# Kernel optimization log

Hardware: AMD Instinct MI355X
Metric: run time of the kernel (lower is better)

The kernel has to match this reference:

```python
import jax, jax.numpy as jnp
import numpy as np

N = 8192      # n_nodes == nfeat (square feature matrix, required by final Linear)
NHID = 64
NCLASS = 8
E = N * 32    # avg degree 32


def setup_inputs() -> dict:
    key = jax.random.key(0)
    ks = jax.random.split(key, 12)
    s = 1.0 / np.sqrt(NHID)
    return {
        "x": jax.random.normal(ks[0], (N, N), dtype=jnp.float32),
        "adj_row": jax.random.randint(ks[1], (E,), 0, N, dtype=jnp.int32),
        "adj_col": jax.random.randint(ks[2], (E,), 0, N, dtype=jnp.int32),
        "adj_val": jax.random.uniform(ks[3], (E,), dtype=jnp.float32),
        "W1": jax.random.uniform(ks[4], (N, NHID), minval=-s, maxval=s, dtype=jnp.float32),
        "b1": jax.random.uniform(ks[5], (NHID,), minval=-s, maxval=s, dtype=jnp.float32),
        "W2": jax.random.uniform(ks[6], (NHID, NHID), minval=-s, maxval=s, dtype=jnp.float32),
        "b2": jax.random.uniform(ks[7], (NHID,), minval=-s, maxval=s, dtype=jnp.float32),
        "W3": jax.random.uniform(ks[8], (NHID, NCLASS), minval=-s, maxval=s, dtype=jnp.float32),
        "b3": jax.random.uniform(ks[9], (NCLASS,), minval=-s, maxval=s, dtype=jnp.float32),
        "Wlin": jax.random.normal(ks[10], (1, N), dtype=jnp.float32) * (1.0 / np.sqrt(N)),
        "blin": jax.random.normal(ks[11], (1,), dtype=jnp.float32) * 0.01,
    }


def _gcn_layer(h, W, b, row, col, val):
    # support = h @ W ; out = spmm(adj, support) + b
    support = h @ W                              # [N, F_out]
    msgs = val[:, None] * support[col]           # gather source rows, scale by edge value
    out = jax.ops.segment_sum(msgs, row, num_segments=N)  # scatter-add into dest rows
    return out + b


def reference(x, adj_row, adj_col, adj_val, W1, b1, W2, b2, W3, b3, Wlin, blin):
    h = jax.nn.relu(_gcn_layer(x, W1, b1, adj_row, adj_col, adj_val))
    # dropout inactive (eval mode)
    h = jax.nn.relu(_gcn_layer(h, W2, b2, adj_row, adj_col, adj_val))
    h = _gcn_layer(h, W3, b3, adj_row, adj_col, adj_val)   # [N, NCLASS]
    h = jax.nn.log_softmax(h, axis=1)
    # LinearLayer(nfeat->1) applied to h^T [NCLASS, N] -> [NCLASS, 1], then transpose
    y = h.T @ Wlin.T + blin                      # [NCLASS, 1]
    return y.T                                   # [1, NCLASS]
```

## Files before the change

### kernel.cpp

```cpp
#include <hip/hip_runtime.h>

#define NN 8192
#define NHID 64
#define NCLASS 8
#define NEDGE (NN * 32)
#define NSPLIT 8
#define DEGCAP 128

typedef __attribute__((ext_vector_type(8))) short bf16x8_t;
typedef __attribute__((ext_vector_type(4))) float f32x4_t;

__device__ __forceinline__ unsigned short f2bf(float f) {
    unsigned int u = __float_as_uint(f);
    u += 0x7FFF + ((u >> 16) & 1);
    return (unsigned short)(u >> 16);
}

__global__ __launch_bounds__(256) void prep_kernel(const float* __restrict__ W1,
                                                   unsigned short* __restrict__ w1t,
                                                   const int* __restrict__ row,
                                                   const int* __restrict__ col,
                                                   const float* __restrict__ val,
                                                   int* __restrict__ cnt,
                                                   int* __restrict__ ccol,
                                                   float* __restrict__ cval) {
    const int bid = blockIdx.x;
    if (bid < 2048) {
        const int idx = bid * 256 + threadIdx.x;
        const int n = idx >> 13;
        const int k = idx & (NN - 1);
        w1t[idx] = f2bf(W1[(size_t)k * NHID + n]);
    } else {
        const int e = (bid - 2048) * 256 + threadIdx.x;
        const int r = row[e];
        const int pos = atomicAdd(&cnt[r], 1);
        if (pos < DEGCAP) {
            ccol[r * DEGCAP + pos] = col[e];
            cval[r * DEGCAP + pos] = val[e];
        }
    }
}

__global__ __launch_bounds__(256, 2) void gemm1_kernel(const float* __restrict__ x,
                                                       const unsigned short* __restrict__ w1t,
                                                       float* __restrict__ part) {
    __shared__ short As[128][72];
    __shared__ short Bs[64][72];
    const int tid = threadIdx.x;
    const int r0 = blockIdx.x * 128;
    const int k0base = blockIdx.y * (NN / NSPLIT);
    const int lane = tid & 63;
    const int wv = tid >> 6;
    const int m16 = lane & 15;
    const int quad = lane >> 4;
    const int c4 = tid & 15;
    const int rA = tid >> 4;
    const int NT = (NN / NSPLIT) / 64;

    f32x4_t acc[2][4];
#pragma unroll
    for (int i = 0; i < 2; ++i)
#pragma unroll
        for (int j = 0; j < 4; ++j) acc[i][j] = (f32x4_t){0.f, 0.f, 0.f, 0.f};

    float4 areg[8];
    uint4 breg[2];
    {
        const int k0 = k0base;
#pragma unroll
        for (int i = 0; i < 8; ++i)
            areg[i] = *(const float4*)(x + (size_t)(r0 + rA + i * 16) * NN + k0 + c4 * 4);
#pragma unroll
        for (int it = 0; it < 2; ++it) {
            const int idx = tid + it * 256;
            breg[it] = *(const uint4*)(w1t + (size_t)(idx >> 3) * NN + k0 + (idx & 7) * 8);
        }
    }

    for (int kt = 0; kt < NT; ++kt) {
#pragma unroll
        for (int i = 0; i < 8; ++i) {
            const int r = rA + i * 16;
            *(ushort4*)(&As[r][c4 * 4]) = make_ushort4(
                f2bf(areg[i].x), f2bf(areg[i].y), f2bf(areg[i].z), f2bf(areg[i].w));
        }
#pragma unroll
        for (int it = 0; it < 2; ++it) {
            const int idx = tid + it * 256;
            *(uint4*)(&Bs[idx >> 3][(idx & 7) * 8]) = breg[it];
        }
        __syncthreads();
        if (kt + 1 < NT) {
            const int k0 = k0base + (kt + 1) * 64;
#pragma unroll
            for (int i = 0; i < 8; ++i)
                areg[i] = *(const float4*)(x + (size_t)(r0 + rA + i * 16) * NN + k0 + c4 * 4);
#pragma unroll
            for (int it = 0; it < 2; ++it) {
                const int idx = tid + it * 256;
                breg[it] = *(const uint4*)(w1t + (size_t)(idx >> 3) * NN + k0 + (idx & 7) * 8);
            }
        }
#pragma unroll
        for (int kk = 0; kk < 64; kk += 32) {
            bf16x8_t af[2], bfr[4];
#pragma unroll
            for (int rt = 0; rt < 2; ++rt)
                af[rt] = *(const bf16x8_t*)(&As[wv * 32 + rt * 16 + m16][kk + quad * 8]);
#pragma unroll
            for (int ct = 0; ct < 4; ++ct)
                bfr[ct] = *(const bf16x8_t*)(&Bs[ct * 16 + m16][kk + quad * 8]);
#pragma unroll
            for (int rt = 0; rt < 2; ++rt)
#pragma unroll
                for (int ct = 0; ct < 4; ++ct)
                    acc[rt][ct] = __builtin_amdgcn_mfma_f32_16x16x32_bf16(
                        af[rt], bfr[ct], acc[rt][ct], 0, 0, 0);
        }
        __syncthreads();
    }
    float* op = part + (size_t)blockIdx.y * (NN * NHID);
#pragma unroll
    for (int rt = 0; rt < 2; ++rt)
#pragma unroll
        for (int ct = 0; ct < 4; ++ct)
#pragma unroll
            for (int reg = 0; reg < 4; ++reg) {
                const int row = r0 + wv * 32 + rt * 16 + quad * 4 + reg;
                const int col = ct * 16 + m16;
                op[(size_t)row * NHID + col] = acc[rt][ct][reg];
            }
}

__global__ __launch_bounds__(256) void reduce8_kernel(const float* __restrict__ part,
                                                      float* __restrict__ sup) {
    const int i = blockIdx.x * 256 + threadIdx.x;
    const float4* p4 = (const float4*)part;
    float4 a = p4[i];
#pragma unroll
    for (int s = 1; s < NSPLIT; ++s) {
        const float4 b = p4[i + (size_t)s * (NN * NHID / 4)];
        a.x += b.x; a.y += b.y; a.z += b.z; a.w += b.w;
    }
    ((float4*)sup)[i] = a;
}

__global__ __launch_bounds__(256) void spmmA_kernel(const float* __restrict__ sup,
                                                    const int* __restrict__ cnt,
                                                    const int* __restrict__ ccol,
                                                    const float* __restrict__ cval,
                                                    const float* __restrict__ b1,
                                                    const float* __restrict__ W2,
                                                    float* __restrict__ s2out) {
    __shared__ float Ws[NHID * NHID];
    for (int i = threadIdx.x; i < NHID * NHID; i += 256) Ws[i] = W2[i];
    __syncthreads();
    const int wid = (blockIdx.x * 256 + threadIdx.x) >> 6;
    const int lane = threadIdx.x & 63;
    const int deg = cnt[wid];
    const int base = wid * DEGCAP;
    float acc = 0.f;
    int i = 0;
    for (; i + 4 <= deg; i += 4) {
        const int4 cc = *(const int4*)(ccol + base + i);
        const float4 vv = *(const float4*)(cval + base + i);
        const float g0 = sup[(size_t)cc.x * NHID + lane];
        const float g1 = sup[(size_t)cc.y * NHID + lane];
        const float g2 = sup[(size_t)cc.z * NHID + lane];
        const float g3 = sup[(size_t)cc.w * NHID + lane];
        acc = fmaf(vv.x, g0, acc);
        acc = fmaf(vv.y, g1, acc);
        acc = fmaf(vv.z, g2, acc);
        acc = fmaf(vv.w, g3, acc);
    }
    for (; i < deg; ++i)
        acc = fmaf(cval[base + i], sup[(size_t)ccol[base + i] * NHID + lane], acc);
    acc = fmaxf(acc + b1[lane], 0.f);
    float o = 0.f;
#pragma unroll
    for (int k = 0; k < NHID; ++k)
        o = fmaf(__shfl(acc, k, 64), Ws[k * NHID + lane], o);
    s2out[(size_t)wid * NHID + lane] = o;
}

__global__ __launch_bounds__(256) void spmmB_kernel(const float* __restrict__ s2,
                                                    const int* __restrict__ cnt,
                                                    const int* __restrict__ ccol,
                                                    const float* __restrict__ cval,
                                                    const float* __restrict__ b2,
                                                    const float* __restrict__ W3,
                                                    float* __restrict__ s3out) {
    const int wid = (blockIdx.x * 256 + threadIdx.x) >> 6;
    const int lane = threadIdx.x & 63;
    const float4 w3a = *(const float4*)(W3 + lane * NCLASS);
    const float4 w3b = *(const float4*)(W3 + lane * NCLASS + 4);
    const int deg = cnt[wid];
    const int base = wid * DEGCAP;
    float acc = 0.f;
    int i = 0;
    for (; i + 4 <= deg; i += 4) {
        const int4 cc = *(const int4*)(ccol + base + i);
        const float4 vv = *(const float4*)(cval + base + i);
        const float g0 = s2[(size_t)cc.x * NHID + lane];
        const float g1 = s2[(size_t)cc.y * NHID + lane];
        const float g2 = s2[(size_t)cc.z * NHID + lane];
        const float g3 = s2[(size_t)cc.w * NHID + lane];
        acc = fmaf(vv.x, g0, acc);
        acc = fmaf(vv.y, g1, acc);
        acc = fmaf(vv.z, g2, acc);
        acc = fmaf(vv.w, g3, acc);
    }
    for (; i < deg; ++i)
        acc = fmaf(cval[base + i], s2[(size_t)ccol[base + i] * NHID + lane], acc);
    acc = fmaxf(acc + b2[lane], 0.f);
    float p[8] = {acc * w3a.x, acc * w3a.y, acc * w3a.z, acc * w3a.w,
                  acc * w3b.x, acc * w3b.y, acc * w3b.z, acc * w3b.w};
#pragma unroll
    for (int off = 32; off > 0; off >>= 1)
#pragma unroll
        for (int c = 0; c < 8; ++c) p[c] += __shfl_down(p[c], off, 64);
    if (lane == 0) {
        float4 r0 = {p[0], p[1], p[2], p[3]};
        float4 r1 = {p[4], p[5], p[6], p[7]};
        *(float4*)(s3out + (size_t)wid * NCLASS) = r0;
        *(float4*)(s3out + (size_t)wid * NCLASS + 4) = r1;
    }
}

__global__ __launch_bounds__(256) void tail_kernel(const float* __restrict__ s3,
                                                   const int* __restrict__ cnt,
                                                   const int* __restrict__ ccol,
                                                   const float* __restrict__ cval,
                                                   const float* __restrict__ b3,
                                                   const float* __restrict__ wlin,
                                                   const float* __restrict__ blin,
                                                   float* __restrict__ outp) {
    __shared__ float cls[4 * NCLASS];
    const int gid = blockIdx.x * 256 + threadIdx.x;
    const int r = gid >> 3;
    const int c = gid & 7;
    const int deg = cnt[r];
    const int base = r * DEGCAP;
    float acc = 0.f;
    int i = 0;
    for (; i + 4 <= deg; i += 4) {
        const int4 cc = *(const int4*)(ccol + base + i);
        const float4 vv = *(const float4*)(cval + base + i);
        const float g0 = s3[(size_t)cc.x * NCLASS + c];
        const float g1 = s3[(size_t)cc.y * NCLASS + c];
        const float g2 = s3[(size_t)cc.z * NCLASS + c];
        const float g3 = s3[(size_t)cc.w * NCLASS + c];
        acc = fmaf(vv.x, g0, acc);
        acc = fmaf(vv.y, g1, acc);
        acc = fmaf(vv.z, g2, acc);
        acc = fmaf(vv.w, g3, acc);
    }
    for (; i < deg; ++i)
        acc = fmaf(cval[base + i], s3[(size_t)ccol[base + i] * NCLASS + c], acc);
    acc += b3[c];
    float m = acc;
    m = fmaxf(m, __shfl_xor(m, 1, 8));
    m = fmaxf(m, __shfl_xor(m, 2, 8));
    m = fmaxf(m, __shfl_xor(m, 4, 8));
    float sx = expf(acc - m);
    sx += __shfl_xor(sx, 1, 8);
    sx += __shfl_xor(sx, 2, 8);
    sx += __shfl_xor(sx, 4, 8);
    const float ls = acc - m - logf(sx);
    float p = ls * wlin[r];
    p += __shfl_xor(p, 8, 64);
    p += __shfl_xor(p, 16, 64);
    p += __shfl_xor(p, 32, 64);
    const int wv = threadIdx.x >> 6;
    if ((threadIdx.x & 63) < 8) cls[wv * NCLASS + c] = p;
    __syncthreads();
    if (threadIdx.x < NCLASS) {
        float v = cls[threadIdx.x] + cls[NCLASS + threadIdx.x] +
                  cls[2 * NCLASS + threadIdx.x] + cls[3 * NCLASS + threadIdx.x];
        if (blockIdx.x == 0) v += blin[0];
        atomicAdd(&outp[threadIdx.x], v);
    }
}

extern "C" void kernel_launch(void* const* d_in, const int* in_sizes, int n_in,
                              void* d_out, int out_size, void* d_ws, size_t ws_size,
                              hipStream_t stream) {
    const float* x       = (const float*)d_in[0];
    const int*   adj_row = (const int*)d_in[1];
    const int*   adj_col = (const int*)d_in[2];
    const float* adj_val = (const float*)d_in[3];
    const float* W1      = (const float*)d_in[4];
    const float* b1      = (const float*)d_in[5];
    const float* W2      = (const float*)d_in[6];
    const float* b2      = (const float*)d_in[7];
    const float* W3      = (const float*)d_in[8];
    const float* b3      = (const float*)d_in[9];
    const float* Wlin    = (const float*)d_in[10];
    const float* blin    = (const float*)d_in[11];
    float* outp = (float*)d_out;

    char* ws = (char*)d_ws;
    float*          part = (float*)ws;
    float*          sup  = (float*)(ws + (16u << 20));
    float*          s2   = (float*)(ws + (18u << 20));
    float*          s3   = (float*)(ws + (20u << 20));
    unsigned short* w1t  = (unsigned short*)(ws + (21u << 20));
    int*            ccol = (int*)(ws + (22u << 20));
    float*          cval = (float*)(ws + (26u << 20));
    int*            cnt  = (int*)(ws + (30u << 20));

    hipMemsetAsync(cnt, 0, (size_t)NN * sizeof(int), stream);
    hipMemsetAsync(outp, 0, NCLASS * sizeof(float), stream);

    prep_kernel<<<3072, 256, 0, stream>>>(W1, w1t, adj_row, adj_col, adj_val,
                                          cnt, ccol, cval);
    gemm1_kernel<<<dim3(NN / 128, NSPLIT), 256, 0, stream>>>(x, w1t, part);
    reduce8_kernel<<<(NN * NHID / 4) / 256, 256, 0, stream>>>(part, sup);
    spmmA_kernel<<<(NN * 64) / 256, 256, 0, stream>>>(sup, cnt, ccol, cval, b1, W2, s2);
    spmmB_kernel<<<(NN * 64) / 256, 256, 0, stream>>>(s2, cnt, ccol, cval, b2, W3, s3);
    tail_kernel<<<(NN * 8) / 256, 256, 0, stream>>>(s3, cnt, ccol, cval, b3,
                                                    Wlin, blin, outp);
}
```

Measured before the change: 483.3 us.

## Fuse all GCN stages into one cooperative persistent kernel with grid barriers

Replaces the six separate kernel launches and two memsets with a single cooperative kernel of 512 blocks. The stages are separated by a software grid barrier built on atomics, and a chain of separate launches is kept as a fallback. The goal is to remove launch gaps and memset overhead between stages. In exchange the sparse stages must loop four rows per warp, and the whole kernel runs at the GEMM's occupancy limit. The CSR build now overlaps with the GEMM inside the same phase, before the barrier that follows it.

```diff
diff --git a/kernel.cpp b/kernel.cpp
--- a/kernel.cpp
+++ b/kernel.cpp
@@ -6,6 +6,8 @@
 #define NEDGE (NN * 32)
 #define NSPLIT 8
 #define DEGCAP 128
+#define GRID 512
+#define GTHREADS (GRID * 256)
 
 typedef __attribute__((ext_vector_type(8))) short bf16x8_t;
 typedef __attribute__((ext_vector_type(4))) float f32x4_t;
@@ -16,22 +18,48 @@
     return (unsigned short)(u >> 16);
 }
 
-__global__ __launch_bounds__(256) void prep_kernel(const float* __restrict__ W1,
-                                                   unsigned short* __restrict__ w1t,
-                                                   const int* __restrict__ row,
-                                                   const int* __restrict__ col,
-                                                   const float* __restrict__ val,
-                                                   int* __restrict__ cnt,
-                                                   int* __restrict__ ccol,
-                                                   float* __restrict__ cval) {
-    const int bid = blockIdx.x;
-    if (bid < 2048) {
-        const int idx = bid * 256 + threadIdx.x;
+__device__ __forceinline__ void gbar(int* count, int* gen) {
+    __syncthreads();
+    if (threadIdx.x == 0) {
+        const int g = __hip_atomic_load(gen, __ATOMIC_RELAXED, __HIP_MEMORY_SCOPE_AGENT);
+        __threadfence();
+        const int arrived =
+            __hip_atomic_fetch_add(count, 1, __ATOMIC_ACQ_REL, __HIP_MEMORY_SCOPE_AGENT);
+        if (arrived == (int)gridDim.x - 1) {
+            __hip_atomic_store(count, 0, __ATOMIC_RELAXED, __HIP_MEMORY_SCOPE_AGENT);
+            __hip_atomic_fetch_add(gen, 1, __ATOMIC_ACQ_REL, __HIP_MEMORY_SCOPE_AGENT);
+        } else {
+            while (__hip_atomic_load(gen, __ATOMIC_ACQUIRE, __HIP_MEMORY_SCOPE_AGENT) == g)
+                __builtin_amdgcn_s_sleep(1);
+        }
+        __threadfence();
+    }
+    __syncthreads();
+}
+
+__device__ __forceinline__ void phase_prep0(int gtid, const float* __restrict__ W1,
+                                            unsigned short* __restrict__ w1t,
+                                            int* __restrict__ cnt,
+                                            float* __restrict__ outp) {
+    if (gtid < NN) cnt[gtid] = 0;
+    if (gtid < NCLASS) outp[gtid] = 0.f;
+#pragma unroll
+    for (int j = 0; j < 4; ++j) {
+        const int idx = j * GTHREADS + gtid;
         const int n = idx >> 13;
         const int k = idx & (NN - 1);
         w1t[idx] = f2bf(W1[(size_t)k * NHID + n]);
-    } else {
-        const int e = (bid - 2048) * 256 + threadIdx.x;
+    }
+}
+
+__device__ __forceinline__ void phase_csr(int gtid, const int* __restrict__ row,
+                                          const int* __restrict__ col,
+                                          const float* __restrict__ val,
+                                          int* __restrict__ cnt, int* __restrict__ ccol,
+                                          float* __restrict__ cval) {
+#pragma unroll
+    for (int j = 0; j < 2; ++j) {
+        const int e = j * GTHREADS + gtid;
         const int r = row[e];
         const int pos = atomicAdd(&cnt[r], 1);
         if (pos < DEGCAP) {
@@ -41,14 +69,14 @@
     }
 }
 
-__global__ __launch_bounds__(256, 2) void gemm1_kernel(const float* __restrict__ x,
-                                                       const unsigned short* __restrict__ w1t,
-                                                       float* __restrict__ part) {
-    __shared__ short As[128][72];
-    __shared__ short Bs[64][72];
+__device__ __forceinline__ void phase_gemm1(const float* __restrict__ x,
+                                            const unsigned short* __restrict__ w1t,
+                                            float* __restrict__ part,
+                                            short (*As)[72], short (*Bs)[72]) {
     const int tid = threadIdx.x;
-    const int r0 = blockIdx.x * 128;
-    const int k0base = blockIdx.y * (NN / NSPLIT);
+    const int r0 = (blockIdx.x >> 3) * 128;
+    const int ksplit = blockIdx.x & 7;
+    const int k0base = ksplit * (NN / NSPLIT);
     const int lane = tid & 63;
     const int wv = tid >> 6;
     const int m16 = lane & 15;
@@ -119,7 +147,7 @@
         }
         __syncthreads();
     }
-    float* op = part + (size_t)blockIdx.y * (NN * NHID);
+    float* op = part + (size_t)ksplit * (NN * NHID);
 #pragma unroll
     for (int rt = 0; rt < 2; ++rt)
 #pragma unroll
@@ -132,110 +160,115 @@
             }
 }
 
-__global__ __launch_bounds__(256) void reduce8_kernel(const float* __restrict__ part,
-                                                      float* __restrict__ sup) {
-    const int i = blockIdx.x * 256 + threadIdx.x;
+__device__ __forceinline__ void phase_reduce(int gtid, const float* __restrict__ part,
+                                             float* __restrict__ sup) {
     const float4* p4 = (const float4*)part;
-    float4 a = p4[i];
+    float4 a = p4[gtid];
 #pragma unroll
     for (int s = 1; s < NSPLIT; ++s) {
-        const float4 b = p4[i + (size_t)s * (NN * NHID / 4)];
+        const float4 b = p4[gtid + (size_t)s * (NN * NHID / 4)];
         a.x += b.x; a.y += b.y; a.z += b.z; a.w += b.w;
     }
-    ((float4*)sup)[i] = a;
-}
-
-__global__ __launch_bounds__(256) void spmmA_kernel(const float* __restrict__ sup,
-                                                    const int* __restrict__ cnt,
-                                                    const int* __restrict__ ccol,
-                                                    const float* __restrict__ cval,
-                                                    const float* __restrict__ b1,
-                                                    const float* __restrict__ W2,
-                                                    float* __restrict__ s2out) {
-    __shared__ float Ws[NHID * NHID];
+    ((float4*)sup)[gtid] = a;
+}
+
+__device__ __forceinline__ void phase_spmmA(const float* __restrict__ sup,
+                                            const int* __restrict__ cnt,
+                                            const int* __restrict__ ccol,
+                                            const float* __restrict__ cval,
+                                            const float* __restrict__ b1,
+                                            const float* __restrict__ W2,
+                                            float* __restrict__ s2out, float* Ws) {
     for (int i = threadIdx.x; i < NHID * NHID; i += 256) Ws[i] = W2[i];
     __syncthreads();
-    const int wid = (blockIdx.x * 256 + threadIdx.x) >> 6;
+    const int gw = (blockIdx.x * 256 + threadIdx.x) >> 6;
     const int lane = threadIdx.x & 63;
-    const int deg = cnt[wid];
-    const int base = wid * DEGCAP;
-    float acc = 0.f;
-    int i = 0;
-    for (; i + 4 <= deg; i += 4) {
-        const int4 cc = *(const int4*)(ccol + base + i);
-        const float4 vv = *(const float4*)(cval + base + i);
-        const float g0 = sup[(size_t)cc.x * NHID + lane];
-        const float g1 = sup[(size_t)cc.y * NHID + lane];
-        const float g2 = sup[(size_t)cc.z * NHID + lane];
-        const float g3 = sup[(size_t)cc.w * NHID + lane];
-        acc = fmaf(vv.x, g0, acc);
-        acc = fmaf(vv.y, g1, acc);
-        acc = fmaf(vv.z, g2, acc);
-        acc = fmaf(vv.w, g3, acc);
-    }
-    for (; i < deg; ++i)
-        acc = fmaf(cval[base + i], sup[(size_t)ccol[base + i] * NHID + lane], acc);
-    acc = fmaxf(acc + b1[lane], 0.f);
-    float o = 0.f;
-#pragma unroll
-    for (int k = 0; k < NHID; ++k)
-        o = fmaf(__shfl(acc, k, 64), Ws[k * NHID + lane], o);
-    s2out[(size_t)wid * NHID + lane] = o;
-}
-
-__global__ __launch_bounds__(256) void spmmB_kernel(const float* __restrict__ s2,
-                                                    const int* __restrict__ cnt,
-                                                    const int* __restrict__ ccol,
-                                                    const float* __restrict__ cval,
-                                                    const float* __restrict__ b2,
-                                                    const float* __restrict__ W3,
-                                                    float* __restrict__ s3out) {
-    const int wid = (blockIdx.x * 256 + threadIdx.x) >> 6;
+    const float bb = b1[lane];
+    for (int rr = 0; rr < 4; ++rr) {
+        const int wid = gw + rr * 2048;
+        const int deg = cnt[wid];
+        const int base = wid * DEGCAP;
+        float acc = 0.f;
+        int i = 0;
+        for (; i + 4 <= deg; i += 4) {
+            const int4 cc = *(const int4*)(ccol + base + i);
+            const float4 vv = *(const float4*)(cval + base + i);
+            const float g0 = sup[(size_t)cc.x * NHID + lane];
+            const float g1 = sup[(size_t)cc.y * NHID + lane];
+            const float g2 = sup[(size_t)cc.z * NHID + lane];
+            const float g3 = sup[(size_t)cc.w * NHID + lane];
+            acc = fmaf(vv.x, g0, acc);
+            acc = fmaf(vv.y, g1, acc);
+            acc = fmaf(vv.z, g2, acc);
+            acc = fmaf(vv.w, g3, acc);
+        }
+        for (; i < deg; ++i)
+            acc = fmaf(cval[base + i], sup[(size_t)ccol[base + i] * NHID + lane], acc);
+        acc = fmaxf(acc + bb, 0.f);
+        float o = 0.f;
+#pragma unroll
+        for (int k = 0; k < NHID; ++k)
+            o = fmaf(__shfl(acc, k, 64), Ws[k * NHID + lane], o);
+        s2out[(size_t)wid * NHID + lane] = o;
+    }
+}
+
+__device__ __forceinline__ void phase_spmmB(const float* __restrict__ s2,
+                                            const int* __restrict__ cnt,
+                                            const int* __restrict__ ccol,
+                                            const float* __restrict__ cval,
+                                            const float* __restrict__ b2,
+                                            const float* __restrict__ W3,
+                                            float* __restrict__ s3out) {
+    const int gw = (blockIdx.x * 256 + threadIdx.x) >> 6;
     const int lane = threadIdx.x & 63;
     const float4 w3a = *(const float4*)(W3 + lane * NCLASS);
     const float4 w3b = *(const float4*)(W3 + lane * NCLASS + 4);
-    const int deg = cnt[wid];
-    const int base = wid * DEGCAP;
-    float acc = 0.f;
-    int i = 0;
-    for (; i + 4 <= deg; i += 4) {
-        const int4 cc = *(const int4*)(ccol + base + i);
-        const float4 vv = *(const float4*)(cval + base + i);
-        const float g0 = s2[(size_t)cc.x * NHID + lane];
-        const float g1 = s2[(size_t)cc.y * NHID + lane];
-        const float g2 = s2[(size_t)cc.z * NHID + lane];
-        const float g3 = s2[(size_t)cc.w * NHID + lane];
-        acc = fmaf(vv.x, g0, acc);
-        acc = fmaf(vv.y, g1, acc);
-        acc = fmaf(vv.z, g2, acc);
-        acc = fmaf(vv.w, g3, acc);
-    }
-    for (; i < deg; ++i)
-        acc = fmaf(cval[base + i], s2[(size_t)ccol[base + i] * NHID + lane], acc);
-    acc = fmaxf(acc + b2[lane], 0.f);
-    float p[8] = {acc * w3a.x, acc * w3a.y, acc * w3a.z, acc * w3a.w,
-                  acc * w3b.x, acc * w3b.y, acc * w3b.z, acc * w3b.w};
-#pragma unroll
-    for (int off = 32; off > 0; off >>= 1)
-#pragma unroll
-        for (int c = 0; c < 8; ++c) p[c] += __shfl_down(p[c], off, 64);
-    if (lane == 0) {
-        float4 r0 = {p[0], p[1], p[2], p[3]};
-        float4 r1 = {p[4], p[5], p[6], p[7]};
-        *(float4*)(s3out + (size_t)wid * NCLASS) = r0;
-        *(float4*)(s3out + (size_t)wid * NCLASS + 4) = r1;
-    }
-}
-
-__global__ __launch_bounds__(256) void tail_kernel(const float* __restrict__ s3,
-                                                   const int* __restrict__ cnt,
-                                                   const int* __restrict__ ccol,
-                                                   const float* __restrict__ cval,
-                                                   const float* __restrict__ b3,
-                                                   const float* __restrict__ wlin,
-                                                   const float* __restrict__ blin,
-                                                   float* __restrict__ outp) {
-    __shared__ float cls[4 * NCLASS];
+    const float bb = b2[lane];
+    for (int rr = 0; rr < 4; ++rr) {
+        const int wid = gw + rr * 2048;
+        const int deg = cnt[wid];
+        const int base = wid * DEGCAP;
+        float acc = 0.f;
+        int i = 0;
+        for (; i + 4 <= deg; i += 4) {
+            const int4 cc = *(const int4*)(ccol + base + i);
+            const float4 vv = *(const float4*)(cval + base + i);
+            const float g0 = s2[(size_t)cc.x * NHID + lane];
+            const float g1 = s2[(size_t)cc.y * NHID + lane];
+            const float g2 = s2[(size_t)cc.z * NHID + lane];
+            const float g3 = s2[(size_t)cc.w * NHID + lane];
+            acc = fmaf(vv.x, g0, acc);
+            acc = fmaf(vv.y, g1, acc);
+            acc = fmaf(vv.z, g2, acc);
+            acc = fmaf(vv.w, g3, acc);
+        }
+        for (; i < deg; ++i)
+            acc = fmaf(cval[base + i], s2[(size_t)ccol[base + i] * NHID + lane], acc);
+        acc = fmaxf(acc + bb, 0.f);
+        float p[8] = {acc * w3a.x, acc * w3a.y, acc * w3a.z, acc * w3a.w,
+                      acc * w3b.x, acc * w3b.y, acc * w3b.z, acc * w3b.w};
+#pragma unroll
+        for (int off = 32; off > 0; off >>= 1)
+#pragma unroll
+            for (int c = 0; c < 8; ++c) p[c] += __shfl_down(p[c], off, 64);
+        if (lane == 0) {
+            float4 r0 = {p[0], p[1], p[2], p[3]};
+            float4 r1 = {p[4], p[5], p[6], p[7]};
+            *(float4*)(s3out + (size_t)wid * NCLASS) = r0;
+            *(float4*)(s3out + (size_t)wid * NCLASS + 4) = r1;
+        }
+    }
+}
+
+__device__ __forceinline__ void phase_tail(const float* __restrict__ s3,
+                                           const int* __restrict__ cnt,
+                                           const int* __restrict__ ccol,
+                                           const float* __restrict__ cval,
+                                           const float* __restrict__ b3,
+                                           const float* __restrict__ wlin,
+                                           const float* __restrict__ blin,
+                                           float* __restrict__ outp, float* cls) {
     const int gid = blockIdx.x * 256 + threadIdx.x;
     const int r = gid >> 3;
     const int c = gid & 7;
@@ -282,6 +315,67 @@
     }
 }
 
+__global__ __launch_bounds__(256, 2) void mega_kernel(
+        const float* x, const int* adj_row, const int* adj_col, const float* adj_val,
+        const float* W1, const float* b1, const float* W2, const float* b2,
+        const float* W3, const float* b3, const float* wlin, const float* blin,
+        float* outp, float* part, float* sup, float* s2, float* s3,
+        unsigned short* w1t, int* ccol, float* cval, int* cnt, int* bar) {
+    __shared__ union {
+        struct { short As[128][72]; short Bs[64][72]; } g;
+        struct { float Ws[NHID * NHID]; float cls[4 * NCLASS]; } s;
+    } u;
+    const int gtid = blockIdx.x * 256 + threadIdx.x;
+    phase_prep0(gtid, W1, w1t, cnt, outp);
+    gbar(bar, bar + 1);
+    phase_csr(gtid, adj_row, adj_col, adj_val, cnt, ccol, cval);
+    phase_gemm1(x, w1t, part, u.g.As, u.g.Bs);
+    gbar(bar, bar + 1);
+    phase_reduce(gtid, part, sup);
+    gbar(bar, bar + 1);
+    phase_spmmA(sup, cnt, ccol, cval, b1, W2, s2, u.s.Ws);
+    gbar(bar, bar + 1);
+    phase_spmmB(s2, cnt, ccol, cval, b2, W3, s3);
+    gbar(bar, bar + 1);
+    if (blockIdx.x < 256) phase_tail(s3, cnt, ccol, cval, b3, wlin, blin, outp, u.s.cls);
+}
+
+__global__ __launch_bounds__(256) void k_prep0(const float* W1, unsigned short* w1t,
+                                               int* cnt, float* outp) {
+    phase_prep0(blockIdx.x * 256 + threadIdx.x, W1, w1t, cnt, outp);
+}
+__global__ __launch_bounds__(256) void k_csr(const int* row, const int* col, const float* val,
+                                             int* cnt, int* ccol, float* cval) {
+    phase_csr(blockIdx.x * 256 + threadIdx.x, row, col, val, cnt, ccol, cval);
+}
+__global__ __launch_bounds__(256, 2) void k_gemm1(const float* x, const unsigned short* w1t,
+                                                  float* part) {
+    __shared__ short As[128][72];
+    __shared__ short Bs[64][72];
+    phase_gemm1(x, w1t, part, As, Bs);
+}
+__global__ __launch_bounds__(256) void k_reduce(const float* part, float* sup) {
+    phase_reduce(blockIdx.x * 256 + threadIdx.x, part, sup);
+}
+__global__ __launch_bounds__(256) void k_spmmA(const float* sup, const int* cnt, const int* ccol,
+                                               const float* cval, const float* b1,
+                                               const float* W2, float* s2) {
+    __shared__ float Ws[NHID * NHID];
+    phase_spmmA(sup, cnt, ccol, cval, b1, W2, s2, Ws);
+}
+__global__ __launch_bounds__(256) void k_spmmB(const float* s2, const int* cnt, const int* ccol,
+                                               const float* cval, const float* b2,
+                                               const float* W3, float* s3) {
+    phase_spmmB(s2, cnt, ccol, cval, b2, W3, s3);
+}
+__global__ __launch_bounds__(256) void k_tail(const float* s3, const int* cnt, const int* ccol,
+                                              const float* cval, const float* b3,
+                                              const float* wlin, const float* blin,
+                                              float* outp) {
+    __shared__ float cls[4 * NCLASS];
+    phase_tail(s3, cnt, ccol, cval, b3, wlin, blin, outp, cls);
+}
+
 extern "C" void kernel_launch(void* const* d_in, const int* in_sizes, int n_in,
                               void* d_out, int out_size, void* d_ws, size_t ws_size,
                               hipStream_t stream) {
@@ -308,16 +402,26 @@
     int*            ccol = (int*)(ws + (22u << 20));
     float*          cval = (float*)(ws + (26u << 20));
     int*            cnt  = (int*)(ws + (30u << 20));
-
-    hipMemsetAsync(cnt, 0, (size_t)NN * sizeof(int), stream);
-    hipMemsetAsync(outp, 0, NCLASS * sizeof(float), stream);
-
-    prep_kernel<<<3072, 256, 0, stream>>>(W1, w1t, adj_row, adj_col, adj_val,
-                                          cnt, ccol, cval);
-    gemm1_kernel<<<dim3(NN / 128, NSPLIT), 256, 0, stream>>>(x, w1t, part);
-    reduce8_kernel<<<(NN * NHID / 4) / 256, 256, 0, stream>>>(part, sup);
-    spmmA_kernel<<<(NN * 64) / 256, 256, 0, stream>>>(sup, cnt, ccol, cval, b1, W2, s2);
-    spmmB_kernel<<<(NN * 64) / 256, 256, 0, stream>>>(s2, cnt, ccol, cval, b2, W3, s3);
-    tail_kernel<<<(NN * 8) / 256, 256, 0, stream>>>(s3, cnt, ccol, cval, b3,
-                                                    Wlin, blin, outp);
-}
+    int*            bar  = (int*)(ws + (31u << 20));
+
+    hipMemsetAsync(bar, 0, 2 * sizeof(int), stream);
+
+    void* kargs[] = {
+        (void*)&x, (void*)&adj_row, (void*)&adj_col, (void*)&adj_val,
+        (void*)&W1, (void*)&b1, (void*)&W2, (void*)&b2, (void*)&W3, (void*)&b3,
+        (void*)&Wlin, (void*)&blin, (void*)&outp,
+        (void*)&part, (void*)&sup, (void*)&s2, (void*)&s3,
+        (void*)&w1t, (void*)&ccol, (void*)&cval, (void*)&cnt, (void*)&bar};
+    hipError_t err = hipLaunchCooperativeKernel((void*)mega_kernel, dim3(GRID), dim3(256),
+                                                kargs, 0, stream);
+    if (err != hipSuccess) {
+        (void)hipGetLastError();
+        k_prep0<<<GRID, 256, 0, stream>>>(W1, w1t, cnt, outp);
+        k_csr<<<GRID, 256, 0, stream>>>(adj_row, adj_col, adj_val, cnt, ccol, cval);
+        k_gemm1<<<GRID, 256, 0, stream>>>(x, w1t, part);
+        k_reduce<<<GRID, 256, 0, stream>>>(part, sup);
+        k_spmmA<<<GRID, 256, 0, stream>>>(sup, cnt, ccol, cval, b1, W2, s2);
+        k_spmmB<<<GRID, 256, 0, stream>>>(s2, cnt, ccol, cval, b2, W3, s3);
+        k_tail<<<256, 256, 0, stream>>>(s3, cnt, ccol, cval, b3, Wlin, blin, outp);
+    }
+}
```

Measured after the change: 971.4 us. 2.01x slower.

## Load GEMM operands directly into MFMA fragments, dropping LDS staging, split K 16 ways

Applied to the files above, without the earlier changes.

The first GEMM no longer stages x and W1ᵀ tiles through shared memory with barriers. Each lane loads its MFMA fragment straight from global memory, converts it to bf16 in registers and prefetches the next K step. K is split 16 ways instead of 8 and the occupancy hint is raised, so more blocks are in flight to hide memory latency on the 256MB x read. In exchange, each wave loads the W1ᵀ fragments itself with no sharing across waves. The partial-sum buffer and the reduction pass also double in size, and the workspace offsets move to make room.

```diff
diff --git a/kernel.cpp b/kernel.cpp
--- a/kernel.cpp
+++ b/kernel.cpp
@@ -4,7 +4,7 @@
 #define NHID 64
 #define NCLASS 8
 #define NEDGE (NN * 32)
-#define NSPLIT 8
+#define NSPLIT 16
 #define DEGCAP 128
 
 typedef __attribute__((ext_vector_type(8))) short bf16x8_t;
@@ -14,6 +14,21 @@
     unsigned int u = __float_as_uint(f);
     u += 0x7FFF + ((u >> 16) & 1);
     return (unsigned short)(u >> 16);
+}
+
+__device__ __forceinline__ bf16x8_t pack8(const float4 lo, const float4 hi) {
+    bf16x8_t r;
+    r[0] = (short)f2bf(lo.x); r[1] = (short)f2bf(lo.y);
+    r[2] = (short)f2bf(lo.z); r[3] = (short)f2bf(lo.w);
+    r[4] = (short)f2bf(hi.x); r[5] = (short)f2bf(hi.y);
+    r[6] = (short)f2bf(hi.z); r[7] = (short)f2bf(hi.w);
+    return r;
+}
+
+__device__ __forceinline__ bf16x8_t as_bf8(const uint4 u) {
+    union { uint4 u; bf16x8_t v; } c;
+    c.u = u;
+    return c.v;
 }
 
 __global__ __launch_bounds__(256) void prep_kernel(const float* __restrict__ W1,
@@ -41,21 +56,21 @@
     }
 }
 
-__global__ __launch_bounds__(256, 2) void gemm1_kernel(const float* __restrict__ x,
+__global__ __launch_bounds__(256, 4) void gemm1_kernel(const float* __restrict__ x,
                                                        const unsigned short* __restrict__ w1t,
                                                        float* __restrict__ part) {
-    __shared__ short As[128][72];
-    __shared__ short Bs[64][72];
     const int tid = threadIdx.x;
     const int r0 = blockIdx.x * 128;
-    const int k0base = blockIdx.y * (NN / NSPLIT);
+    const int k0 = blockIdx.y * (NN / NSPLIT);
     const int lane = tid & 63;
     const int wv = tid >> 6;
     const int m16 = lane & 15;
     const int quad = lane >> 4;
-    const int c4 = tid & 15;
-    const int rA = tid >> 4;
-    const int NT = (NN / NSPLIT) / 64;
+    const int NT = (NN / NSPLIT) / 32;
+
+    const float* xr0 = x + (size_t)(r0 + wv * 32 + m16) * NN + k0 + quad * 8;
+    const float* xr1 = xr0 + (size_t)16 * NN;
+    const unsigned short* bp = w1t + (size_t)m16 * NN + k0 + quad * 8;
 
     f32x4_t acc[2][4];
 #pragma unroll
@@ -63,61 +78,42 @@
 #pragma unroll
         for (int j = 0; j < 4; ++j) acc[i][j] = (f32x4_t){0.f, 0.f, 0.f, 0.f};
 
-    float4 areg[8];
-    uint4 breg[2];
-    {
-        const int k0 = k0base;
-#pragma unroll
-        for (int i = 0; i < 8; ++i)
-            areg[i] = *(const float4*)(x + (size_t)(r0 + rA + i * 16) * NN + k0 + c4 * 4);
-#pragma unroll
-        for (int it = 0; it < 2; ++it) {
-            const int idx = tid + it * 256;
-            breg[it] = *(const uint4*)(w1t + (size_t)(idx >> 3) * NN + k0 + (idx & 7) * 8);
+    float4 a0l = *(const float4*)(xr0);
+    float4 a0h = *(const float4*)(xr0 + 4);
+    float4 a1l = *(const float4*)(xr1);
+    float4 a1h = *(const float4*)(xr1 + 4);
+    uint4 b0 = *(const uint4*)(bp);
+    uint4 b1 = *(const uint4*)(bp + (size_t)16 * NN);
+    uint4 b2 = *(const uint4*)(bp + (size_t)32 * NN);
+    uint4 b3 = *(const uint4*)(bp + (size_t)48 * NN);
+
+#pragma unroll 2
+    for (int kt = 0; kt < NT; ++kt) {
+        const bf16x8_t af0 = pack8(a0l, a0h);
+        const bf16x8_t af1 = pack8(a1l, a1h);
+        const bf16x8_t bf0 = as_bf8(b0);
+        const bf16x8_t bf1 = as_bf8(b1);
+        const bf16x8_t bf2 = as_bf8(b2);
+        const bf16x8_t bf3 = as_bf8(b3);
+        if (kt + 1 < NT) {
+            const int o = (kt + 1) * 32;
+            a0l = *(const float4*)(xr0 + o);
+            a0h = *(const float4*)(xr0 + o + 4);
+            a1l = *(const float4*)(xr1 + o);
+            a1h = *(const float4*)(xr1 + o + 4);
+            b0 = *(const uint4*)(bp + o);
+            b1 = *(const uint4*)(bp + o + (size_t)16 * NN);
+            b2 = *(const uint4*)(bp + o + (size_t)32 * NN);
+            b3 = *(const uint4*)(bp + o + (size_t)48 * NN);
         }
-    }
-
-    for (int kt = 0; kt < NT; ++kt) {
-#pragma unroll
-        for (int i = 0; i < 8; ++i) {
-            const int r = rA + i * 16;
-            *(ushort4*)(&As[r][c4 * 4]) = make_ushort4(
-                f2bf(areg[i].x), f2bf(areg[i].y), f2bf(areg[i].z), f2bf(areg[i].w));
-        }
-#pragma unroll
-        for (int it = 0; it < 2; ++it) {
-            const int idx = tid + it * 256;
-            *(uint4*)(&Bs[idx >> 3][(idx & 7) * 8]) = breg[it];
-        }
-        __syncthreads();
-        if (kt + 1 < NT) {
-            const int k0 = k0base + (kt + 1) * 64;
-#pragma unroll
-            for (int i = 0; i < 8; ++i)
-                areg[i] = *(const float4*)(x + (size_t)(r0 + rA + i * 16) * NN + k0 + c4 * 4);
-#pragma unroll
-            for (int it = 0; it < 2; ++it) {
-                const int idx = tid + it * 256;
-                breg[it] = *(const uint4*)(w1t + (size_t)(idx >> 3) * NN + k0 + (idx & 7) * 8);
-            }
-        }
-#pragma unroll
-        for (int kk = 0; kk < 64; kk += 32) {
-            bf16x8_t af[2], bfr[4];
-#pragma unroll
-            for (int rt = 0; rt < 2; ++rt)
-                af[rt] = *(const bf16x8_t*)(&As[wv * 32 + rt * 16 + m16][kk + quad * 8]);
-#pragma unroll
-            for (int ct = 0; ct < 4; ++ct)
-                bfr[ct] = *(const bf16x8_t*)(&Bs[ct * 16 + m16][kk + quad * 8]);
-#pragma unroll
-            for (int rt = 0; rt < 2; ++rt)
-#pragma unroll
-                for (int ct = 0; ct < 4; ++ct)
-                    acc[rt][ct] = __builtin_amdgcn_mfma_f32_16x16x32_bf16(
-                        af[rt], bfr[ct], acc[rt][ct], 0, 0, 0);
-        }
-        __syncthreads();
+        acc[0][0] = __builtin_amdgcn_mfma_f32_16x16x32_bf16(af0, bf0, acc[0][0], 0, 0, 0);
+        acc[0][1] = __builtin_amdgcn_mfma_f32_16x16x32_bf16(af0, bf1, acc[0][1], 0, 0, 0);
+        acc[0][2] = __builtin_amdgcn_mfma_f32_16x16x32_bf16(af0, bf2, acc[0][2], 0, 0, 0);
+        acc[0][3] = __builtin_amdgcn_mfma_f32_16x16x32_bf16(af0, bf3, acc[0][3], 0, 0, 0);
+        acc[1][0] = __builtin_amdgcn_mfma_f32_16x16x32_bf16(af1, bf0, acc[1][0], 0, 0, 0);
+        acc[1][1] = __builtin_amdgcn_mfma_f32_16x16x32_bf16(af1, bf1, acc[1][1], 0, 0, 0);
+        acc[1][2] = __builtin_amdgcn_mfma_f32_16x16x32_bf16(af1, bf2, acc[1][2], 0, 0, 0);
+        acc[1][3] = __builtin_amdgcn_mfma_f32_16x16x32_bf16(af1, bf3, acc[1][3], 0, 0, 0);
     }
     float* op = part + (size_t)blockIdx.y * (NN * NHID);
 #pragma unroll
@@ -132,8 +128,8 @@
             }
 }
 
-__global__ __launch_bounds__(256) void reduce8_kernel(const float* __restrict__ part,
-                                                      float* __restrict__ sup) {
+__global__ __launch_bounds__(256) void reduce_kernel(const float* __restrict__ part,
+                                                     float* __restrict__ sup) {
     const int i = blockIdx.x * 256 + threadIdx.x;
     const float4* p4 = (const float4*)part;
     float4 a = p4[i];
@@ -301,13 +297,13 @@
 
     char* ws = (char*)d_ws;
     float*          part = (float*)ws;
-    float*          sup  = (float*)(ws + (16u << 20));
-    float*          s2   = (float*)(ws + (18u << 20));
-    float*          s3   = (float*)(ws + (20u << 20));
-    unsigned short* w1t  = (unsigned short*)(ws + (21u << 20));
-    int*            ccol = (int*)(ws + (22u << 20));
-    float*          cval = (float*)(ws + (26u << 20));
-    int*            cnt  = (int*)(ws + (30u << 20));
+    float*          sup  = (float*)(ws + (32u << 20));
+    float*          s2   = (float*)(ws + (34u << 20));
+    float*          s3   = (float*)(ws + (36u << 20));
+    unsigned short* w1t  = (unsigned short*)(ws + (37u << 20));
+    int*            ccol = (int*)(ws + (38u << 20));
+    float*          cval = (float*)(ws + (42u << 20));
+    int*            cnt  = (int*)(ws + (46u << 20));
 
     hipMemsetAsync(cnt, 0, (size_t)NN * sizeof(int), stream);
     hipMemsetAsync(outp, 0, NCLASS * sizeof(float), stream);
@@ -315,7 +311,7 @@
     prep_kernel<<<3072, 256, 0, stream>>>(W1, w1t, adj_row, adj_col, adj_val,
                                           cnt, ccol, cval);
     gemm1_kernel<<<dim3(NN / 128, NSPLIT), 256, 0, stream>>>(x, w1t, part);
-    reduce8_kernel<<<(NN * NHID / 4) / 256, 256, 0, stream>>>(part, sup);
+    reduce_kernel<<<(NN * NHID / 4) / 256, 256, 0, stream>>>(part, sup);
     spmmA_kernel<<<(NN * 64) / 256, 256, 0, stream>>>(sup, cnt, ccol, cval, b1, W2, s2);
     spmmB_kernel<<<(NN * 64) / 256, 256, 0, stream>>>(s2, cnt, ccol, cval, b2, W3, s3);
     tail_kernel<<<(NN * 8) / 256, 256, 0, stream>>>(s3, cnt, ccol, cval, b3,
```

New measurement: 473.2 us. 2.1% less time.
